# Kernel optimization log

Measured on AMD Instinct MI355X. Metric: run time of the kernel, lower is better.

The kernel has to match this reference:

```python
import jax, jax.numpy as jnp
import numpy as np

V, G, K, B = 2048, 48, 128, 1024


def setup_inputs() -> dict:
    key = jax.random.key(0)
    k_idx, k_emb = jax.random.split(key, 2)
    # one-hot input words: B x V
    word_idx = jax.random.randint(k_idx, (B,), 0, V)
    inp = jax.nn.one_hot(word_idx, V, dtype=jnp.float32)
    # |G| dense V x V permutation matrices (symmetry_group.index2inverse[i])
    rng = np.random.RandomState(0)
    perm_idx = np.stack([rng.permutation(V) for _ in range(G)])  # [G, V]
    perms = jax.nn.one_hot(jnp.asarray(perm_idx), V, dtype=jnp.float32)  # [G, V, V]
    # embedding table V x K
    emb = jax.random.normal(k_emb, (V, K), dtype=jnp.float32) * 0.02
    return {"input": inp, "perms": perms, "emb": emb}


def reference(input, perms, emb):
    # permute_word: stack([word @ index2inverse[i] for i in range(|G|)], dim=1)
    scores = jnp.einsum('bv,gvw->bgw', input, perms)  # [B, G, V]
    # argmax over vocab recovers the permuted index
    permutation_indices = jnp.argmax(scores, axis=-1)  # [B, G]
    # embedding gather, then squeeze (no-op for B > 1)
    return jnp.squeeze(emb[permutation_indices])  # [B, G, K]
```

## Files before the change

kernel.cpp:

```cpp
#include <hip/hip_runtime.h>

#define V 2048
#define G 48
#define K 128
#define B 1024


__global__ void zero_needed(int* __restrict__ needed) {
    int i = blockIdx.x * blockDim.x + threadIdx.x;
    if (i < V) needed[i] = 0;
}

__global__ void find_word_idx(const float* __restrict__ input,
                              int* __restrict__ word_idx,
                              int* __restrict__ needed) {
    int b = blockIdx.x;
    int t = threadIdx.x;
    const float* row = input + (size_t)b * V;
    int base = t * 8;
    float4 x0 = *(const float4*)(row + base);
    float4 x1 = *(const float4*)(row + base + 4);
    int hit = -1;
    if      (x0.x > 0.5f) hit = base + 0;
    else if (x0.y > 0.5f) hit = base + 1;
    else if (x0.z > 0.5f) hit = base + 2;
    else if (x0.w > 0.5f) hit = base + 3;
    else if (x1.x > 0.5f) hit = base + 4;
    else if (x1.y > 0.5f) hit = base + 5;
    else if (x1.z > 0.5f) hit = base + 6;
    else if (x1.w > 0.5f) hit = base + 7;
    if (hit >= 0) {
        word_idx[b] = hit;
        needed[hit] = 1;
    }
}

__global__ void scan_perms(const float* __restrict__ perms,
                           const int* __restrict__ needed,
                           int* __restrict__ tab) {
    int wid  = (blockIdx.x * blockDim.x + threadIdx.x) >> 6;
    int lane = threadIdx.x & 63;
    if (wid >= G * V) return;
    int g = wid >> 11;
    int v = wid & (V - 1);
    if (!needed[v]) return;
    const float* row = perms + ((size_t)g * V + (size_t)v) * V;
    for (int it = 0; it < 8; ++it) {
        int base = it * 256 + lane * 4;
        float4 x = *(const float4*)(row + base);
        int hit = -1;
        if      (x.x > 0.5f) hit = base + 0;
        else if (x.y > 0.5f) hit = base + 1;
        else if (x.z > 0.5f) hit = base + 2;
        else if (x.w > 0.5f) hit = base + 3;
        if (hit >= 0) tab[wid] = hit;
        if (__any(hit >= 0)) break;
    }
}

__global__ void gather_emb(const float* __restrict__ emb,
                           const int* __restrict__ word_idx,
                           const int* __restrict__ tab,
                           float* __restrict__ out) {
    int pair = blockIdx.x * 8 + (threadIdx.x >> 5);
    int lane = threadIdx.x & 31;
    int b = pair / G;
    int g = pair - b * G;
    int w = word_idx[b];
    int idx = tab[g * V + w];
    float4 val = *(const float4*)(emb + (size_t)idx * K + lane * 4);
    *(float4*)(out + (size_t)pair * K + lane * 4) = val;
}

extern "C" void kernel_launch(void* const* d_in, const int* in_sizes, int n_in,
                              void* d_out, int out_size, void* d_ws, size_t ws_size,
                              hipStream_t stream) {
    const float* input = (const float*)d_in[0];
    const float* perms = (const float*)d_in[1];
    const float* emb   = (const float*)d_in[2];
    float* out = (float*)d_out;

    int* ws       = (int*)d_ws;
    int* word_idx = ws;
    int* needed   = ws + B;
    int* tab      = ws + B + V;

    zero_needed<<<(V + 255) / 256, 256, 0, stream>>>(needed);
    find_word_idx<<<B, 256, 0, stream>>>(input, word_idx, needed);
    scan_perms<<<(G * V) / 4, 256, 0, stream>>>(perms, needed, tab);
    gather_emb<<<(B * G) / 8, 256, 0, stream>>>(emb, word_idx, tab, out);
}
```

Baseline: 922.1 us.

## Fuse permutation scan with embedding gather per batch-group pair

Replaces the deduplicated per-(group,word) permutation scan, table write and separate gather kernel with one kernel where each wavefront scans the permutation row for its (group,batch) word and directly copies the embedding row. This removes two launches, the needed-mask zeroing and the intermediate table round trip, and avoids launching waves that exit immediately. In exchange, repeated words are scanned redundantly, so total scan work rises somewhat.

```diff
diff --git a/kernel.cpp b/kernel.cpp
--- a/kernel.cpp
+++ b/kernel.cpp
@@ -6,14 +6,8 @@
 #define B 1024
 
 
-__global__ void zero_needed(int* __restrict__ needed) {
-    int i = blockIdx.x * blockDim.x + threadIdx.x;
-    if (i < V) needed[i] = 0;
-}
-
 __global__ void find_word_idx(const float* __restrict__ input,
-                              int* __restrict__ word_idx,
-                              int* __restrict__ needed) {
+                              int* __restrict__ word_idx) {
     int b = blockIdx.x;
     int t = threadIdx.x;
     const float* row = input + (size_t)b * V;
@@ -29,22 +23,21 @@
     else if (x1.y > 0.5f) hit = base + 5;
     else if (x1.z > 0.5f) hit = base + 6;
     else if (x1.w > 0.5f) hit = base + 7;
-    if (hit >= 0) {
-        word_idx[b] = hit;
-        needed[hit] = 1;
-    }
+    if (hit >= 0) word_idx[b] = hit;
 }
 
-__global__ void scan_perms(const float* __restrict__ perms,
-                           const int* __restrict__ needed,
-                           int* __restrict__ tab) {
-    int wid  = (blockIdx.x * blockDim.x + threadIdx.x) >> 6;
+__global__ void scan_and_gather(const float* __restrict__ perms,
+                                const float* __restrict__ emb,
+                                const int* __restrict__ word_idx,
+                                float* __restrict__ out) {
+    int wid  = blockIdx.x * 4 + (threadIdx.x >> 6);
     int lane = threadIdx.x & 63;
-    if (wid >= G * V) return;
-    int g = wid >> 11;
-    int v = wid & (V - 1);
-    if (!needed[v]) return;
-    const float* row = perms + ((size_t)g * V + (size_t)v) * V;
+    int g = wid >> 10;
+    int b = wid & (B - 1);
+    int w = word_idx[b];
+    const float* row = perms + ((size_t)g * V + (size_t)w) * V;
+
+    int idx = -1;
     for (int it = 0; it < 8; ++it) {
         int base = it * 256 + lane * 4;
         float4 x = *(const float4*)(row + base);
@@ -53,23 +46,16 @@
         else if (x.y > 0.5f) hit = base + 1;
         else if (x.z > 0.5f) hit = base + 2;
         else if (x.w > 0.5f) hit = base + 3;
-        if (hit >= 0) tab[wid] = hit;
-        if (__any(hit >= 0)) break;
+        unsigned long long m = __ballot(hit >= 0);
+        if (m) {
+            int src = (int)__builtin_ctzll(m);
+            idx = __shfl(hit, src);
+            break;
+        }
     }
-}
 
-__global__ void gather_emb(const float* __restrict__ emb,
-                           const int* __restrict__ word_idx,
-                           const int* __restrict__ tab,
-                           float* __restrict__ out) {
-    int pair = blockIdx.x * 8 + (threadIdx.x >> 5);
-    int lane = threadIdx.x & 31;
-    int b = pair / G;
-    int g = pair - b * G;
-    int w = word_idx[b];
-    int idx = tab[g * V + w];
-    float4 val = *(const float4*)(emb + (size_t)idx * K + lane * 4);
-    *(float4*)(out + (size_t)pair * K + lane * 4) = val;
+    float2 e = *(const float2*)(emb + (size_t)idx * K + lane * 2);
+    *(float2*)(out + ((size_t)b * G + g) * K + lane * 2) = e;
 }
 
 extern "C" void kernel_launch(void* const* d_in, const int* in_sizes, int n_in,
@@ -80,13 +66,8 @@
     const float* emb   = (const float*)d_in[2];
     float* out = (float*)d_out;
 
-    int* ws       = (int*)d_ws;
-    int* word_idx = ws;
-    int* needed   = ws + B;
-    int* tab      = ws + B + V;
+    int* word_idx = (int*)d_ws;
 
-    zero_needed<<<(V + 255) / 256, 256, 0, stream>>>(needed);
-    find_word_idx<<<B, 256, 0, stream>>>(input, word_idx, needed);
-    scan_perms<<<(G * V) / 4, 256, 0, stream>>>(perms, needed, tab);
-    gather_emb<<<(B * G) / 8, 256, 0, stream>>>(emb, word_idx, tab, out);
+    find_word_idx<<<B, 256, 0, stream>>>(input, word_idx);
+    scan_and_gather<<<(G * B) / 4, 256, 0, stream>>>(perms, emb, word_idx, out);
 }
```

Result: no change. 911.2 us (-1.2%).
